# Kernel tuning notes

Hardware: AMD Instinct MI355X
Metric: run time of the kernel (lower is better)

Reference implementation:

```python
import jax, jax.numpy as jnp
import numpy as np

B, N, F, D, H, T = 32, 1024, 32, 64, 64, 4


def setup_inputs() -> dict:
    key = jax.random.key(0)
    ks = jax.random.split(key, 12)
    def w(k, shape):
        return 0.01 * jax.random.normal(k, shape, dtype=jnp.float32)
    z = lambda *s: jnp.zeros(s, jnp.float32)
    return {
        "xv": jax.random.normal(ks[0], (B, N, F), dtype=jnp.float32),
        "option": jax.random.uniform(ks[1], (B, 1), dtype=jnp.float32),
        "adj": jax.random.normal(ks[2], (N, N), dtype=jnp.float32),
        "mu1": w(ks[3], (F, D)),
        "W2": w(ks[4], (D, D)), "b2": z(D),
        "W3": w(ks[5], (D, D)), "b3": z(D),
        "W4": w(ks[6], (D, 1)), "b4": z(D),
        "Wq1": w(ks[7], (D, D)), "bq1": z(D),
        "Wq2": w(ks[8], (D, 1)), "bq2": z(D),
        "Wreg": w(ks[9], (H, 2 * D)), "breg": z(H),
        "Wq": w(ks[10], (1, H)), "bq": z(1),
    }


def reference(xv, option, adj, mu1, W2, b2, W3, b3, W4, b4,
              Wq1, bq1, Wq2, bq2, Wreg, breg, Wq, bq):
    # binary adjacency for message passing, raw weights for the mu_4 branch
    A = (adj > 0).astype(xv.dtype)                       # [N,N]
    mu_1 = jnp.maximum(xv @ mu1, 0.0)                    # [B,N,D]
    # mu_4: Linear(1,D) over every edge weight, clamp, sum over neighbors
    # (identical value every round t>=1, so computed once)
    mu4 = jnp.maximum(adj[..., None] * W4[:, 0] + b4, 0.0).sum(axis=1)[None]  # [1,N,D]
    mu3 = mu4 @ W3.T + b3                                # [1,N,D]
    mu = mu_1                                            # t = 0
    for _ in range(1, T):                                # t = 1..T-1
        mu_pool = jnp.einsum('nm,bmd->bnd', A, mu)       # neighbor aggregation
        mu2 = mu_pool @ W2.T + b2
        mu = jnp.maximum(mu_1 + mu2 + mu3, 0.0)
    mu_mean = jnp.maximum(mu.mean(axis=1, keepdims=True) @ Wq1.T + bq1, 0.0)  # [B,1,D]
    mu_aug = jnp.concatenate([mu, mu_mean], axis=1)      # [B,N+1,D]
    q2 = option.reshape(B, 1, 1) @ Wq2.T + bq2           # [B,1,D]
    q2 = jnp.broadcast_to(q2, (B, N + 1, D))
    q_ = jnp.concatenate([mu_aug, q2], axis=-1)          # [B,N+1,2D]
    qreg = jnp.maximum(q_ @ Wreg.T + breg, 0.0)          # [B,N+1,H]
    return qreg @ Wq.T + bq                              # [B,N+1,1]
```

## Files before the change

### kernel.cpp

```cpp
#include <hip/hip_runtime.h>
#include <hip/hip_bf16.h>

#define Bc 32
#define Nc 1024
#define Fc 32
#define Dc 64
#define Hc 64

typedef __bf16 bf16;
typedef __bf16 bf16x4 __attribute__((ext_vector_type(4)));
typedef __bf16 bf16x8 __attribute__((ext_vector_type(8)));
typedef float  f32x4  __attribute__((ext_vector_type(4)));

#define AS_STRIDE 136
#define MS_STRIDE 72

#define LDS_RND_NONF 26112
#define LDS_RND_FIN  27904

__global__ void k_pc(const float* __restrict__ adj, const float* __restrict__ W4,
                     const float* __restrict__ b4, const float* __restrict__ W3,
                     const float* __restrict__ b3, const float* __restrict__ b2,
                     const float* __restrict__ W2, const float* __restrict__ option,
                     const float* __restrict__ Wq2, const float* __restrict__ bq2,
                     const float* __restrict__ Wreg, const float* __restrict__ breg,
                     bf16* __restrict__ Abf, float* __restrict__ C3,
                     bf16* __restrict__ W2bf, float* __restrict__ c2base,
                     float* __restrict__ musum) {
    const int t = threadIdx.x;
    if (blockIdx.x < 1024) {
        const int n = blockIdx.x;
        const float* arow = adj + (size_t)n * Nc;
        {
            const float4 a = *(const float4*)&arow[t * 4];
            bf16x4 o;
            o[0] = (bf16)((a.x > 0.f) ? 1.f : 0.f);
            o[1] = (bf16)((a.y > 0.f) ? 1.f : 0.f);
            o[2] = (bf16)((a.z > 0.f) ? 1.f : 0.f);
            o[3] = (bf16)((a.w > 0.f) ? 1.f : 0.f);
            *(bf16x4*)&Abf[(size_t)n * Nc + t * 4] = o;
        }
        const int e = t & 63, g = t >> 6;
        __shared__ float red[256];
        __shared__ float mu4_s[64];
        const float w4e = W4[e], b4e = b4[e];
        float acc = 0.f;
        const float4* arow4 = (const float4*)(arow + g * 256);
#pragma unroll 8
        for (int j = 0; j < 64; ++j) {
            const float4 av = arow4[j];
            acc += fmaxf(fmaf(av.x, w4e, b4e), 0.f);
            acc += fmaxf(fmaf(av.y, w4e, b4e), 0.f);
            acc += fmaxf(fmaf(av.z, w4e, b4e), 0.f);
            acc += fmaxf(fmaf(av.w, w4e, b4e), 0.f);
        }
        red[t] = acc;
        __syncthreads();
        if (g == 0) mu4_s[e] = red[e] + red[64 + e] + red[128 + e] + red[192 + e];
        __syncthreads();
        if (t < 64) {
            const int d = t;
            float a = b3[d] + b2[d];
#pragma unroll
            for (int ee = 0; ee < 64; ++ee) a = fmaf(mu4_s[ee], W3[d * 64 + ee], a);
            C3[n * 64 + d] = a;
        }
    } else {
        for (int j = t * 16; j < t * 16 + 16; ++j) W2bf[j] = (bf16)W2[j];
        for (int i = t; i < 2048; i += 256) musum[i] = 0.f;
        for (int i = t; i < 2048; i += 256) {
            const int b = i >> 6, h = i & 63;
            const float opt = option[b];
            float a = breg[h];
#pragma unroll
            for (int j = 0; j < 64; ++j)
                a = fmaf(fmaf(opt, Wq2[j], bq2[j]), Wreg[h * 128 + 64 + j], a);
            c2base[i] = a;
        }
    }
}

__global__ void k_mu1(const float* __restrict__ xv, const float* __restrict__ w,
                      const bf16* __restrict__ W2bf,
                      float* __restrict__ mu_1, bf16* __restrict__ Xt) {
    const int nb = blockIdx.x, b = blockIdx.y, t = threadIdx.x;
    const int n0 = nb * 64;
    const int l = t & 63, wv = t >> 6, lm = l & 15, q = l >> 4;
    __shared__ bf16 xhi[64 * 40], xlo[64 * 40];
    __shared__ bf16 whi[64 * 40], wlo[64 * 40];
    __shared__ bf16 muS[64 * MS_STRIDE];
    __shared__ bf16 W2s[64 * MS_STRIDE];

    {
        const int row = t >> 2, f0 = (t & 3) * 8;
        const float* src = &xv[((size_t)b * Nc + n0 + row) * Fc + f0];
        const float4 v0 = *(const float4*)src;
        const float4 v1 = *(const float4*)(src + 4);
        bf16x8 hi, lo;
        float vv[8] = {v0.x, v0.y, v0.z, v0.w, v1.x, v1.y, v1.z, v1.w};
#pragma unroll
        for (int j = 0; j < 8; ++j) { hi[j] = (bf16)vv[j]; lo[j] = (bf16)(vv[j] - (float)hi[j]); }
        *(bf16x8*)&xhi[row * 40 + f0] = hi;
        *(bf16x8*)&xlo[row * 40 + f0] = lo;
    }
    {
        const int d = t >> 2, f0 = (t & 3) * 8;
#pragma unroll
        for (int j = 0; j < 8; ++j) {
            const float v = w[(f0 + j) * Dc + d];
            const bf16 hi = (bf16)v;
            whi[d * 40 + f0 + j] = hi;
            wlo[d * 40 + f0 + j] = (bf16)(v - (float)hi);
        }
    }
#pragma unroll
    for (int i = 0; i < 2; ++i) {
        int g = i * 256 + t, row = g >> 3, c = g & 7;
        *(bf16x8*)&W2s[row * MS_STRIDE + c * 8] = *(const bf16x8*)&W2bf[row * 64 + c * 8];
    }
    __syncthreads();

    f32x4 acc[4];
#pragma unroll
    for (int ct = 0; ct < 4; ++ct)
#pragma unroll
        for (int r = 0; r < 4; ++r) acc[ct][r] = 0.f;
    {
        const bf16x8 aHi = *(const bf16x8*)&xhi[(wv * 16 + lm) * 40 + q * 8];
        const bf16x8 aLo = *(const bf16x8*)&xlo[(wv * 16 + lm) * 40 + q * 8];
#pragma unroll
        for (int ct = 0; ct < 4; ++ct) {
            const bf16x8 bHi = *(const bf16x8*)&whi[(ct * 16 + lm) * 40 + q * 8];
            const bf16x8 bLo = *(const bf16x8*)&wlo[(ct * 16 + lm) * 40 + q * 8];
            acc[ct] = __builtin_amdgcn_mfma_f32_16x16x32_bf16(aHi, bHi, acc[ct], 0, 0, 0);
            acc[ct] = __builtin_amdgcn_mfma_f32_16x16x32_bf16(aLo, bHi, acc[ct], 0, 0, 0);
            acc[ct] = __builtin_amdgcn_mfma_f32_16x16x32_bf16(aHi, bLo, acc[ct], 0, 0, 0);
        }
    }
#pragma unroll
    for (int ct = 0; ct < 4; ++ct) {
        const int col = ct * 16 + lm;
#pragma unroll
        for (int r = 0; r < 4; ++r) {
            const int row = wv * 16 + q * 4 + r;
            const float v = fmaxf(acc[ct][r], 0.f);
            mu_1[((size_t)b * Nc + n0 + row) * Dc + col] = v;
            muS[row * MS_STRIDE + col] = (bf16)v;
        }
    }
    __syncthreads();
    f32x4 xacc[4];
#pragma unroll
    for (int ct = 0; ct < 4; ++ct)
#pragma unroll
        for (int r = 0; r < 4; ++r) xacc[ct][r] = 0.f;
#pragma unroll
    for (int s = 0; s < 2; ++s) {
        bf16x8 a = *(const bf16x8*)&muS[(wv * 16 + lm) * MS_STRIDE + s * 32 + q * 8];
#pragma unroll
        for (int ct = 0; ct < 4; ++ct) {
            bf16x8 bv = *(const bf16x8*)&W2s[(ct * 16 + lm) * MS_STRIDE + s * 32 + q * 8];
            xacc[ct] = __builtin_amdgcn_mfma_f32_16x16x32_bf16(a, bv, xacc[ct], 0, 0, 0);
        }
    }
#pragma unroll
    for (int ct = 0; ct < 4; ++ct) {
        const int dd = ct * 16 + lm;
        bf16x4 p;
#pragma unroll
        for (int r = 0; r < 4; ++r) p[r] = (bf16)xacc[ct][r];
        *(bf16x4*)&Xt[(size_t)b * 65536 + (size_t)dd * 1024 + n0 + wv * 16 + q * 4] = p;
    }
}

template <bool FINAL>
__global__ __launch_bounds__(256, 4)
void k_round(const bf16* __restrict__ Abf, const bf16* __restrict__ Xt_in,
             const float* __restrict__ mu_1, const float* __restrict__ C3,
             const bf16* __restrict__ W2bf, bf16* __restrict__ Xt_out,
             const float* __restrict__ Wreg, const float* __restrict__ c2base,
             const float* __restrict__ Wq, const float* __restrict__ bq,
             float* __restrict__ musum, float* __restrict__ out) {
    const int b = blockIdx.x, nb = blockIdx.y, t = threadIdx.x;
    const int n0 = nb * 32;
    const int l = t & 63, wv = t >> 6, lm = l & 15, q = l >> 4;
    const int rw = wv & 1, cth = wv >> 1;
    extern __shared__ char smem[];
    bf16* As   = (bf16*)smem;
    bf16* Xs   = (bf16*)(smem + 8704);
    bf16* muHi = (bf16*)smem;
    bf16* WHi  = (bf16*)(smem + 4608);
    bf16* muLo = (bf16*)(smem + 13824);
    bf16* WLo  = (bf16*)(smem + 18432);
    float* rpart = (float*)(smem + 27648);

    bf16x8 pw[2];
    bf16x4 wrhi[4], wrlo[4];
    if (!FINAL) {
#pragma unroll
        for (int i = 0; i < 2; ++i) {
            int g = i * 256 + t, row = g >> 3, c = g & 7;
            pw[i] = *(const bf16x8*)&W2bf[row * 64 + c * 8];
        }
    } else {
#pragma unroll
        for (int i = 0; i < 4; ++i) {
            int g = i * 1024 + t * 4;
            int h = g >> 6, d = g & 63;
            const float4 w4 = *(const float4*)&Wreg[h * 128 + d];
            wrhi[i][0] = (bf16)w4.x; wrlo[i][0] = (bf16)(w4.x - (float)wrhi[i][0]);
            wrhi[i][1] = (bf16)w4.y; wrlo[i][1] = (bf16)(w4.y - (float)wrhi[i][1]);
            wrhi[i][2] = (bf16)w4.z; wrlo[i][2] = (bf16)(w4.z - (float)wrhi[i][2]);
            wrhi[i][3] = (bf16)w4.w; wrlo[i][3] = (bf16)(w4.w - (float)wrhi[i][3]);
        }
    }

    f32x4 acc[2];
#pragma unroll
    for (int ct = 0; ct < 2; ++ct)
#pragma unroll
        for (int r = 0; r < 4; ++r) acc[ct][r] = 0.f;

    const bf16* Arow = Abf + (size_t)n0 * 1024;
    const bf16* Xrow = Xt_in + (size_t)b * 65536;

    bf16x8 pa[2], px[4];
#pragma unroll
    for (int i = 0; i < 2; ++i) {
        int g = i * 256 + t, row = g >> 4, c = g & 15;
        pa[i] = *(const bf16x8*)&Arow[(size_t)row * 1024 + c * 8];
    }
#pragma unroll
    for (int i = 0; i < 4; ++i) {
        int g = i * 256 + t, row = g >> 4, c = g & 15;
        px[i] = *(const bf16x8*)&Xrow[(size_t)row * 1024 + c * 8];
    }

    for (int kc = 0; kc < 1024; kc += 128) {
        __syncthreads();
#pragma unroll
        for (int i = 0; i < 2; ++i) {
            int g = i * 256 + t, row = g >> 4, c = g & 15;
            *(bf16x8*)&As[row * AS_STRIDE + c * 8] = pa[i];
        }
#pragma unroll
        for (int i = 0; i < 4; ++i) {
            int g = i * 256 + t, row = g >> 4, c = g & 15;
            *(bf16x8*)&Xs[row * AS_STRIDE + c * 8] = px[i];
        }
        __syncthreads();
        if (kc + 128 < 1024) {
#pragma unroll
            for (int i = 0; i < 2; ++i) {
                int g = i * 256 + t, row = g >> 4, c = g & 15;
                pa[i] = *(const bf16x8*)&Arow[(size_t)row * 1024 + kc + 128 + c * 8];
            }
#pragma unroll
            for (int i = 0; i < 4; ++i) {
                int g = i * 256 + t, row = g >> 4, c = g & 15;
                px[i] = *(const bf16x8*)&Xrow[(size_t)row * 1024 + kc + 128 + c * 8];
            }
        }
#pragma unroll
        for (int s = 0; s < 4; ++s) {
            bf16x8 a = *(const bf16x8*)&As[(rw * 16 + lm) * AS_STRIDE + s * 32 + q * 8];
#pragma unroll
            for (int ct = 0; ct < 2; ++ct) {
                bf16x8 bv = *(const bf16x8*)&Xs[(cth * 32 + ct * 16 + lm) * AS_STRIDE + s * 32 + q * 8];
                acc[ct] = __builtin_amdgcn_mfma_f32_16x16x32_bf16(a, bv, acc[ct], 0, 0, 0);
            }
        }
    }

    float vals[2][4];
#pragma unroll
    for (int ct = 0; ct < 2; ++ct) {
        const int col = cth * 32 + ct * 16 + lm;
#pragma unroll
        for (int r = 0; r < 4; ++r) {
            const int n = n0 + rw * 16 + q * 4 + r;
            float v = mu_1[((size_t)b * Nc + n) * Dc + col] + acc[ct][r] + C3[n * 64 + col];
            vals[ct][r] = fmaxf(v, 0.f);
        }
    }

    __syncthreads();
    if (!FINAL) {
#pragma unroll
        for (int i = 0; i < 2; ++i) {
            int g = i * 256 + t, row = g >> 3, c = g & 7;
            *(bf16x8*)&WHi[row * MS_STRIDE + c * 8] = pw[i];
        }
    } else {
#pragma unroll
        for (int i = 0; i < 4; ++i) {
            int g = i * 1024 + t * 4;
            int h = g >> 6, d = g & 63;
            *(bf16x4*)&WHi[h * MS_STRIDE + d] = wrhi[i];
            *(bf16x4*)&WLo[h * MS_STRIDE + d] = wrlo[i];
        }
    }
#pragma unroll
    for (int ct = 0; ct < 2; ++ct) {
        const int col = cth * 32 + ct * 16 + lm;
#pragma unroll
        for (int r = 0; r < 4; ++r) {
            const int row = rw * 16 + q * 4 + r;
            const float v = vals[ct][r];
            const bf16 hi = (bf16)v;
            muHi[row * MS_STRIDE + col] = hi;
            if (FINAL) muLo[row * MS_STRIDE + col] = (bf16)(v - (float)hi);
        }
    }
    if (FINAL) {
#pragma unroll
        for (int ct = 0; ct < 2; ++ct) {
            float s = vals[ct][0] + vals[ct][1] + vals[ct][2] + vals[ct][3];
            s += __shfl_xor(s, 16);
            s += __shfl_xor(s, 32);
            if (q == 0) atomicAdd(&musum[b * 64 + cth * 32 + ct * 16 + lm], s);
        }
    }
    __syncthreads();

    f32x4 xacc[2];
#pragma unroll
    for (int ct = 0; ct < 2; ++ct)
#pragma unroll
        for (int r = 0; r < 4; ++r) xacc[ct][r] = 0.f;

    if (!FINAL) {
#pragma unroll
        for (int s = 0; s < 2; ++s) {
            bf16x8 a = *(const bf16x8*)&muHi[(rw * 16 + lm) * MS_STRIDE + s * 32 + q * 8];
#pragma unroll
            for (int ct = 0; ct < 2; ++ct) {
                bf16x8 bv = *(const bf16x8*)&WHi[(cth * 32 + ct * 16 + lm) * MS_STRIDE + s * 32 + q * 8];
                xacc[ct] = __builtin_amdgcn_mfma_f32_16x16x32_bf16(a, bv, xacc[ct], 0, 0, 0);
            }
        }
#pragma unroll
        for (int ct = 0; ct < 2; ++ct) {
            const int dd = cth * 32 + ct * 16 + lm;
            bf16x4 p;
#pragma unroll
            for (int r = 0; r < 4; ++r) p[r] = (bf16)xacc[ct][r];
            *(bf16x4*)&Xt_out[(size_t)b * 65536 + (size_t)dd * 1024 + n0 + rw * 16 + q * 4] = p;
        }
    } else {
#pragma unroll
        for (int s = 0; s < 2; ++s) {
            const int aoff = (rw * 16 + lm) * MS_STRIDE + s * 32 + q * 8;
            bf16x8 aHi = *(const bf16x8*)&muHi[aoff];
            bf16x8 aLo = *(const bf16x8*)&muLo[aoff];
#pragma unroll
            for (int ct = 0; ct < 2; ++ct) {
                const int boff = (cth * 32 + ct * 16 + lm) * MS_STRIDE + s * 32 + q * 8;
                bf16x8 bHi = *(const bf16x8*)&WHi[boff];
                bf16x8 bLo = *(const bf16x8*)&WLo[boff];
                xacc[ct] = __builtin_amdgcn_mfma_f32_16x16x32_bf16(aHi, bHi, xacc[ct], 0, 0, 0);
                xacc[ct] = __builtin_amdgcn_mfma_f32_16x16x32_bf16(aLo, bHi, xacc[ct], 0, 0, 0);
                xacc[ct] = __builtin_amdgcn_mfma_f32_16x16x32_bf16(aHi, bLo, xacc[ct], 0, 0, 0);
            }
        }
        float rowsum[4] = {0.f, 0.f, 0.f, 0.f};
#pragma unroll
        for (int ct = 0; ct < 2; ++ct) {
            const int h = cth * 32 + ct * 16 + lm;
            const float c2 = c2base[b * 64 + h];
            const float wqh = Wq[h];
#pragma unroll
            for (int r = 0; r < 4; ++r)
                rowsum[r] += fmaxf(xacc[ct][r] + c2, 0.f) * wqh;
        }
#pragma unroll
        for (int r = 0; r < 4; ++r) {
            float v = rowsum[r];
            v += __shfl_xor(v, 1);
            v += __shfl_xor(v, 2);
            v += __shfl_xor(v, 4);
            v += __shfl_xor(v, 8);
            if (lm == 0) rpart[cth * 32 + rw * 16 + q * 4 + r] = v;
        }
        __syncthreads();
        if (t < 32)
            out[(size_t)b * (Nc + 1) + n0 + t] = rpart[t] + rpart[32 + t] + bq[0];
    }
}

__global__ void k_tail(const float* __restrict__ musum, const float* __restrict__ Wq1,
                       const float* __restrict__ bq1, const float* __restrict__ Wreg,
                       const float* __restrict__ c2base, const float* __restrict__ Wq,
                       const float* __restrict__ bq, float* __restrict__ out) {
    const int b = blockIdx.x, l = threadIdx.x;
    __shared__ float mean_s[64];
    __shared__ float mp[64];
    mean_s[l] = musum[b * 64 + l] * (1.f / Nc);
    __syncthreads();
    float a = bq1[l];
#pragma unroll
    for (int e = 0; e < 64; ++e) a = fmaf(mean_s[e], Wq1[l * 64 + e], a);
    mp[l] = fmaxf(a, 0.f);
    __syncthreads();
    float h = c2base[b * 64 + l];
#pragma unroll
    for (int d = 0; d < 64; ++d) h = fmaf(mp[d], Wreg[l * 128 + d], h);
    float v = fmaxf(h, 0.f) * Wq[l];
#pragma unroll
    for (int off = 32; off; off >>= 1) v += __shfl_down(v, off);
    if (l == 0) out[(size_t)b * (Nc + 1) + Nc] = v + bq[0];
}

extern "C" void kernel_launch(void* const* d_in, const int* in_sizes, int n_in,
                              void* d_out, int out_size, void* d_ws, size_t ws_size,
                              hipStream_t stream) {
    const float* xv     = (const float*)d_in[0];
    const float* option = (const float*)d_in[1];
    const float* adj    = (const float*)d_in[2];
    const float* mu1w   = (const float*)d_in[3];
    const float* W2     = (const float*)d_in[4];
    const float* b2     = (const float*)d_in[5];
    const float* W3     = (const float*)d_in[6];
    const float* b3     = (const float*)d_in[7];
    const float* W4     = (const float*)d_in[8];
    const float* b4     = (const float*)d_in[9];
    const float* Wq1    = (const float*)d_in[10];
    const float* bq1    = (const float*)d_in[11];
    const float* Wq2    = (const float*)d_in[12];
    const float* bq2    = (const float*)d_in[13];
    const float* Wreg   = (const float*)d_in[14];
    const float* breg   = (const float*)d_in[15];
    const float* Wq     = (const float*)d_in[16];
    const float* bq     = (const float*)d_in[17];
    float* out = (float*)d_out;

    float* ws = (float*)d_ws;
    const size_t MU = (size_t)Bc * Nc * Dc;
    float* mu_1     = ws;
    float* C3       = ws + MU;
    float* c2base   = C3 + 65536;
    float* musum    = c2base + 2048;
    bf16*  Abf      = (bf16*)(musum + 2048);
    bf16*  W2bf     = Abf + (size_t)Nc * Nc;
    bf16*  Xt0      = W2bf + 4096;
    bf16*  Xt1      = Xt0 + MU;

    k_pc<<<1025, 256, 0, stream>>>(adj, W4, b4, W3, b3, b2, W2, option, Wq2, bq2,
                                   Wreg, breg, Abf, C3, W2bf, c2base, musum);
    k_mu1<<<dim3(Nc / 64, Bc), 256, 0, stream>>>(xv, mu1w, W2bf, mu_1, Xt0);
    k_round<false><<<dim3(Bc, Nc / 32), 256, LDS_RND_NONF, stream>>>(
        Abf, Xt0, mu_1, C3, W2bf, Xt1,
        nullptr, nullptr, nullptr, nullptr, nullptr, nullptr);
    k_round<false><<<dim3(Bc, Nc / 32), 256, LDS_RND_NONF, stream>>>(
        Abf, Xt1, mu_1, C3, W2bf, Xt0,
        nullptr, nullptr, nullptr, nullptr, nullptr, nullptr);
    k_round<true><<<dim3(Bc, Nc / 32), 256, LDS_RND_FIN, stream>>>(
        Abf, Xt0, mu_1, C3, nullptr, nullptr,
        Wreg, c2base, Wq, bq, musum, out);
    k_tail<<<Bc, 64, 0, stream>>>(musum, Wq1, bq1, Wreg, c2base, Wq, bq, out);
}
```

Measured before the change: 159.3 us.

## Drop LDS staging in aggregation GEMM; load MFMA fragments directly with 64-row tiles

The round kernel no longer stages A and X tiles through shared memory with double-buffered register prefetch. Each wave now reads its MFMA fragments straight from global memory and computes a 2x2 block of 16x16 tiles. Block tile height doubles from 32 to 64 rows, which halves the grid and lowers the launch-bounds occupancy hint. The aim is to remove LDS round trips and barriers in the main loop, at the risk of uncoalesced global loads and lower occupancy.

```diff
diff --git a/kernel.cpp b/kernel.cpp
--- a/kernel.cpp
+++ b/kernel.cpp
@@ -12,11 +12,9 @@
 typedef __bf16 bf16x8 __attribute__((ext_vector_type(8)));
 typedef float  f32x4  __attribute__((ext_vector_type(4)));
 
-#define AS_STRIDE 136
-#define MS_STRIDE 72
-
-#define LDS_RND_NONF 26112
-#define LDS_RND_FIN  27904
+#define MS 72
+#define LDS_RND_NONF 18432
+#define LDS_RND_FIN  37376
 
 __global__ void k_pc(const float* __restrict__ adj, const float* __restrict__ W4,
                      const float* __restrict__ b4, const float* __restrict__ W3,
@@ -88,9 +86,8 @@
     const int l = t & 63, wv = t >> 6, lm = l & 15, q = l >> 4;
     __shared__ bf16 xhi[64 * 40], xlo[64 * 40];
     __shared__ bf16 whi[64 * 40], wlo[64 * 40];
-    __shared__ bf16 muS[64 * MS_STRIDE];
-    __shared__ bf16 W2s[64 * MS_STRIDE];
-
+    __shared__ bf16 muS[64 * MS];
+    __shared__ bf16 W2s[64 * MS];
     {
         const int row = t >> 2, f0 = (t & 3) * 8;
         const float* src = &xv[((size_t)b * Nc + n0 + row) * Fc + f0];
@@ -116,10 +113,9 @@
 #pragma unroll
     for (int i = 0; i < 2; ++i) {
         int g = i * 256 + t, row = g >> 3, c = g & 7;
-        *(bf16x8*)&W2s[row * MS_STRIDE + c * 8] = *(const bf16x8*)&W2bf[row * 64 + c * 8];
+        *(bf16x8*)&W2s[row * MS + c * 8] = *(const bf16x8*)&W2bf[row * 64 + c * 8];
     }
     __syncthreads();
-
     f32x4 acc[4];
 #pragma unroll
     for (int ct = 0; ct < 4; ++ct)
@@ -145,7 +141,7 @@
             const int row = wv * 16 + q * 4 + r;
             const float v = fmaxf(acc[ct][r], 0.f);
             mu_1[((size_t)b * Nc + n0 + row) * Dc + col] = v;
-            muS[row * MS_STRIDE + col] = (bf16)v;
+            muS[row * MS + col] = (bf16)v;
         }
     }
     __syncthreads();
@@ -156,10 +152,10 @@
         for (int r = 0; r < 4; ++r) xacc[ct][r] = 0.f;
 #pragma unroll
     for (int s = 0; s < 2; ++s) {
-        bf16x8 a = *(const bf16x8*)&muS[(wv * 16 + lm) * MS_STRIDE + s * 32 + q * 8];
+        bf16x8 a = *(const bf16x8*)&muS[(wv * 16 + lm) * MS + s * 32 + q * 8];
 #pragma unroll
         for (int ct = 0; ct < 4; ++ct) {
-            bf16x8 bv = *(const bf16x8*)&W2s[(ct * 16 + lm) * MS_STRIDE + s * 32 + q * 8];
+            bf16x8 bv = *(const bf16x8*)&W2s[(ct * 16 + lm) * MS + s * 32 + q * 8];
             xacc[ct] = __builtin_amdgcn_mfma_f32_16x16x32_bf16(a, bv, xacc[ct], 0, 0, 0);
         }
     }
@@ -174,7 +170,7 @@
 }
 
 template <bool FINAL>
-__global__ __launch_bounds__(256, 4)
+__global__ __launch_bounds__(256, 2)
 void k_round(const bf16* __restrict__ Abf, const bf16* __restrict__ Xt_in,
              const float* __restrict__ mu_1, const float* __restrict__ C3,
              const bf16* __restrict__ W2bf, bf16* __restrict__ Xt_out,
@@ -182,209 +178,197 @@
              const float* __restrict__ Wq, const float* __restrict__ bq,
              float* __restrict__ musum, float* __restrict__ out) {
     const int b = blockIdx.x, nb = blockIdx.y, t = threadIdx.x;
-    const int n0 = nb * 32;
+    const int n0 = nb * 64;
     const int l = t & 63, wv = t >> 6, lm = l & 15, q = l >> 4;
-    const int rw = wv & 1, cth = wv >> 1;
+    const int rh = wv & 1, ch = wv >> 1;
     extern __shared__ char smem[];
-    bf16* As   = (bf16*)smem;
-    bf16* Xs   = (bf16*)(smem + 8704);
     bf16* muHi = (bf16*)smem;
-    bf16* WHi  = (bf16*)(smem + 4608);
-    bf16* muLo = (bf16*)(smem + 13824);
-    bf16* WLo  = (bf16*)(smem + 18432);
-    float* rpart = (float*)(smem + 27648);
-
-    bf16x8 pw[2];
-    bf16x4 wrhi[4], wrlo[4];
+    bf16* muLo = (bf16*)(smem + 9216);
+    bf16* WHi  = (bf16*)(smem + (FINAL ? 18432 : 9216));
+    bf16* WLo  = (bf16*)(smem + 27648);
+    float* rpart = (float*)(smem + 36864);
+
     if (!FINAL) {
 #pragma unroll
         for (int i = 0; i < 2; ++i) {
             int g = i * 256 + t, row = g >> 3, c = g & 7;
-            pw[i] = *(const bf16x8*)&W2bf[row * 64 + c * 8];
+            *(bf16x8*)&WHi[row * MS + c * 8] = *(const bf16x8*)&W2bf[row * 64 + c * 8];
         }
     } else {
 #pragma unroll
         for (int i = 0; i < 4; ++i) {
-            int g = i * 1024 + t * 4;
-            int h = g >> 6, d = g & 63;
+            int g = i * 1024 + t * 4, h = g >> 6, d = g & 63;
             const float4 w4 = *(const float4*)&Wreg[h * 128 + d];
-            wrhi[i][0] = (bf16)w4.x; wrlo[i][0] = (bf16)(w4.x - (float)wrhi[i][0]);
-            wrhi[i][1] = (bf16)w4.y; wrlo[i][1] = (bf16)(w4.y - (float)wrhi[i][1]);
-            wrhi[i][2] = (bf16)w4.z; wrlo[i][2] = (bf16)(w4.z - (float)wrhi[i][2]);
-            wrhi[i][3] = (bf16)w4.w; wrlo[i][3] = (bf16)(w4.w - (float)wrhi[i][3]);
-        }
-    }
-
-    f32x4 acc[2];
-#pragma unroll
-    for (int ct = 0; ct < 2; ++ct)
-#pragma unroll
-        for (int r = 0; r < 4; ++r) acc[ct][r] = 0.f;
-
-    const bf16* Arow = Abf + (size_t)n0 * 1024;
-    const bf16* Xrow = Xt_in + (size_t)b * 65536;
-
-    bf16x8 pa[2], px[4];
-#pragma unroll
-    for (int i = 0; i < 2; ++i) {
-        int g = i * 256 + t, row = g >> 4, c = g & 15;
-        pa[i] = *(const bf16x8*)&Arow[(size_t)row * 1024 + c * 8];
-    }
-#pragma unroll
-    for (int i = 0; i < 4; ++i) {
-        int g = i * 256 + t, row = g >> 4, c = g & 15;
-        px[i] = *(const bf16x8*)&Xrow[(size_t)row * 1024 + c * 8];
-    }
-
-    for (int kc = 0; kc < 1024; kc += 128) {
-        __syncthreads();
-#pragma unroll
-        for (int i = 0; i < 2; ++i) {
-            int g = i * 256 + t, row = g >> 4, c = g & 15;
-            *(bf16x8*)&As[row * AS_STRIDE + c * 8] = pa[i];
-        }
-#pragma unroll
-        for (int i = 0; i < 4; ++i) {
-            int g = i * 256 + t, row = g >> 4, c = g & 15;
-            *(bf16x8*)&Xs[row * AS_STRIDE + c * 8] = px[i];
-        }
-        __syncthreads();
-        if (kc + 128 < 1024) {
-#pragma unroll
-            for (int i = 0; i < 2; ++i) {
-                int g = i * 256 + t, row = g >> 4, c = g & 15;
-                pa[i] = *(const bf16x8*)&Arow[(size_t)row * 1024 + kc + 128 + c * 8];
-            }
-#pragma unroll
-            for (int i = 0; i < 4; ++i) {
-                int g = i * 256 + t, row = g >> 4, c = g & 15;
-                px[i] = *(const bf16x8*)&Xrow[(size_t)row * 1024 + kc + 128 + c * 8];
-            }
-        }
-#pragma unroll
-        for (int s = 0; s < 4; ++s) {
-            bf16x8 a = *(const bf16x8*)&As[(rw * 16 + lm) * AS_STRIDE + s * 32 + q * 8];
-#pragma unroll
-            for (int ct = 0; ct < 2; ++ct) {
-                bf16x8 bv = *(const bf16x8*)&Xs[(cth * 32 + ct * 16 + lm) * AS_STRIDE + s * 32 + q * 8];
-                acc[ct] = __builtin_amdgcn_mfma_f32_16x16x32_bf16(a, bv, acc[ct], 0, 0, 0);
-            }
-        }
-    }
-
-    float vals[2][4];
-#pragma unroll
-    for (int ct = 0; ct < 2; ++ct) {
-        const int col = cth * 32 + ct * 16 + lm;
-#pragma unroll
-        for (int r = 0; r < 4; ++r) {
-            const int n = n0 + rw * 16 + q * 4 + r;
-            float v = mu_1[((size_t)b * Nc + n) * Dc + col] + acc[ct][r] + C3[n * 64 + col];
-            vals[ct][r] = fmaxf(v, 0.f);
-        }
-    }
-
-    __syncthreads();
-    if (!FINAL) {
-#pragma unroll
-        for (int i = 0; i < 2; ++i) {
-            int g = i * 256 + t, row = g >> 3, c = g & 7;
-            *(bf16x8*)&WHi[row * MS_STRIDE + c * 8] = pw[i];
-        }
-    } else {
-#pragma unroll
-        for (int i = 0; i < 4; ++i) {
-            int g = i * 1024 + t * 4;
-            int h = g >> 6, d = g & 63;
-            *(bf16x4*)&WHi[h * MS_STRIDE + d] = wrhi[i];
-            *(bf16x4*)&WLo[h * MS_STRIDE + d] = wrlo[i];
-        }
-    }
-#pragma unroll
-    for (int ct = 0; ct < 2; ++ct) {
-        const int col = cth * 32 + ct * 16 + lm;
-#pragma unroll
-        for (int r = 0; r < 4; ++r) {
-            const int row = rw * 16 + q * 4 + r;
-            const float v = vals[ct][r];
-            const bf16 hi = (bf16)v;
-            muHi[row * MS_STRIDE + col] = hi;
-            if (FINAL) muLo[row * MS_STRIDE + col] = (bf16)(v - (float)hi);
-        }
-    }
+            bf16x4 ohi, olo;
+            ohi[0] = (bf16)w4.x; olo[0] = (bf16)(w4.x - (float)ohi[0]);
+            ohi[1] = (bf16)w4.y; olo[1] = (bf16)(w4.y - (float)ohi[1]);
+            ohi[2] = (bf16)w4.z; olo[2] = (bf16)(w4.z - (float)ohi[2]);
+            ohi[3] = (bf16)w4.w; olo[3] = (bf16)(w4.w - (float)ohi[3]);
+            *(bf16x4*)&WHi[h * MS + d] = ohi;
+            *(bf16x4*)&WLo[h * MS + d] = olo;
+        }
+    }
+
+    f32x4 acc[2][2];
+#pragma unroll
+    for (int rt = 0; rt < 2; ++rt)
+#pragma unroll
+        for (int ct = 0; ct < 2; ++ct)
+#pragma unroll
+            for (int r = 0; r < 4; ++r) acc[rt][ct][r] = 0.f;
+
+    const bf16* Ab0 = Abf + (size_t)(n0 + rh * 32 + lm) * 1024 + q * 8;
+    const bf16* Ab1 = Ab0 + 16 * 1024;
+    const bf16* Xb0 = Xt_in + (size_t)b * 65536 + (size_t)(ch * 32 + lm) * 1024 + q * 8;
+    const bf16* Xb1 = Xb0 + 16 * 1024;
+#pragma unroll 4
+    for (int s = 0; s < 32; ++s) {
+        const int o = s * 32;
+        bf16x8 a0 = *(const bf16x8*)&Ab0[o];
+        bf16x8 a1 = *(const bf16x8*)&Ab1[o];
+        bf16x8 x0 = *(const bf16x8*)&Xb0[o];
+        bf16x8 x1 = *(const bf16x8*)&Xb1[o];
+        acc[0][0] = __builtin_amdgcn_mfma_f32_16x16x32_bf16(a0, x0, acc[0][0], 0, 0, 0);
+        acc[0][1] = __builtin_amdgcn_mfma_f32_16x16x32_bf16(a0, x1, acc[0][1], 0, 0, 0);
+        acc[1][0] = __builtin_amdgcn_mfma_f32_16x16x32_bf16(a1, x0, acc[1][0], 0, 0, 0);
+        acc[1][1] = __builtin_amdgcn_mfma_f32_16x16x32_bf16(a1, x1, acc[1][1], 0, 0, 0);
+    }
+
+    float vals[2][2][4];
+#pragma unroll
+    for (int rt = 0; rt < 2; ++rt)
+#pragma unroll
+        for (int ct = 0; ct < 2; ++ct) {
+            const int col = ch * 32 + ct * 16 + lm;
+#pragma unroll
+            for (int r = 0; r < 4; ++r) {
+                const int n = n0 + rh * 32 + rt * 16 + q * 4 + r;
+                float v = mu_1[((size_t)b * Nc + n) * Dc + col] + acc[rt][ct][r]
+                        + C3[n * 64 + col];
+                vals[rt][ct][r] = fmaxf(v, 0.f);
+            }
+        }
+
+#pragma unroll
+    for (int rt = 0; rt < 2; ++rt)
+#pragma unroll
+        for (int ct = 0; ct < 2; ++ct) {
+            const int col = ch * 32 + ct * 16 + lm;
+#pragma unroll
+            for (int r = 0; r < 4; ++r) {
+                const int row = rh * 32 + rt * 16 + q * 4 + r;
+                const float v = vals[rt][ct][r];
+                const bf16 hi = (bf16)v;
+                muHi[row * MS + col] = hi;
+                if (FINAL) muLo[row * MS + col] = (bf16)(v - (float)hi);
+            }
+        }
     if (FINAL) {
 #pragma unroll
         for (int ct = 0; ct < 2; ++ct) {
-            float s = vals[ct][0] + vals[ct][1] + vals[ct][2] + vals[ct][3];
+            float s = 0.f;
+#pragma unroll
+            for (int rt = 0; rt < 2; ++rt)
+#pragma unroll
+                for (int r = 0; r < 4; ++r) s += vals[rt][ct][r];
             s += __shfl_xor(s, 16);
             s += __shfl_xor(s, 32);
-            if (q == 0) atomicAdd(&musum[b * 64 + cth * 32 + ct * 16 + lm], s);
+            if (q == 0) atomicAdd(&musum[b * 64 + ch * 32 + ct * 16 + lm], s);
         }
     }
     __syncthreads();
 
-    f32x4 xacc[2];
-#pragma unroll
-    for (int ct = 0; ct < 2; ++ct)
-#pragma unroll
-        for (int r = 0; r < 4; ++r) xacc[ct][r] = 0.f;
+    f32x4 xacc[2][2];
+#pragma unroll
+    for (int rt = 0; rt < 2; ++rt)
+#pragma unroll
+        for (int ct = 0; ct < 2; ++ct)
+#pragma unroll
+            for (int r = 0; r < 4; ++r) xacc[rt][ct][r] = 0.f;
 
     if (!FINAL) {
 #pragma unroll
         for (int s = 0; s < 2; ++s) {
-            bf16x8 a = *(const bf16x8*)&muHi[(rw * 16 + lm) * MS_STRIDE + s * 32 + q * 8];
+            bf16x8 aM[2], bW[2];
+#pragma unroll
+            for (int rt = 0; rt < 2; ++rt)
+                aM[rt] = *(const bf16x8*)&muHi[(rh * 32 + rt * 16 + lm) * MS + s * 32 + q * 8];
+#pragma unroll
+            for (int ct = 0; ct < 2; ++ct)
+                bW[ct] = *(const bf16x8*)&WHi[(ch * 32 + ct * 16 + lm) * MS + s * 32 + q * 8];
+#pragma unroll
+            for (int rt = 0; rt < 2; ++rt)
+#pragma unroll
+                for (int ct = 0; ct < 2; ++ct)
+                    xacc[rt][ct] = __builtin_amdgcn_mfma_f32_16x16x32_bf16(aM[rt], bW[ct],
+                                                                           xacc[rt][ct], 0, 0, 0);
+        }
+#pragma unroll
+        for (int rt = 0; rt < 2; ++rt)
 #pragma unroll
             for (int ct = 0; ct < 2; ++ct) {
-                bf16x8 bv = *(const bf16x8*)&WHi[(cth * 32 + ct * 16 + lm) * MS_STRIDE + s * 32 + q * 8];
-                xacc[ct] = __builtin_amdgcn_mfma_f32_16x16x32_bf16(a, bv, xacc[ct], 0, 0, 0);
-            }
-        }
+                const int dd = ch * 32 + ct * 16 + lm;
+                bf16x4 p;
+#pragma unroll
+                for (int r = 0; r < 4; ++r) p[r] = (bf16)xacc[rt][ct][r];
+                *(bf16x4*)&Xt_out[(size_t)b * 65536 + (size_t)dd * 1024
+                                  + n0 + rh * 32 + rt * 16 + q * 4] = p;
+            }
+    } else {
+#pragma unroll
+        for (int s = 0; s < 2; ++s) {
+            bf16x8 aH[2], aL[2], bH[2], bL[2];
+#pragma unroll
+            for (int rt = 0; rt < 2; ++rt) {
+                const int ao = (rh * 32 + rt * 16 + lm) * MS + s * 32 + q * 8;
+                aH[rt] = *(const bf16x8*)&muHi[ao];
+                aL[rt] = *(const bf16x8*)&muLo[ao];
+            }
+#pragma unroll
+            for (int ct = 0; ct < 2; ++ct) {
+                const int bo = (ch * 32 + ct * 16 + lm) * MS + s * 32 + q * 8;
+                bH[ct] = *(const bf16x8*)&WHi[bo];
+                bL[ct] = *(const bf16x8*)&WLo[bo];
+            }
+#pragma unroll
+            for (int rt = 0; rt < 2; ++rt)
+#pragma unroll
+                for (int ct = 0; ct < 2; ++ct) {
+                    xacc[rt][ct] = __builtin_amdgcn_mfma_f32_16x16x32_bf16(aH[rt], bH[ct],
+                                                                           xacc[rt][ct], 0, 0, 0);
+                    xacc[rt][ct] = __builtin_amdgcn_mfma_f32_16x16x32_bf16(aL[rt], bH[ct],
+                                                                           xacc[rt][ct], 0, 0, 0);
+                    xacc[rt][ct] = __builtin_amdgcn_mfma_f32_16x16x32_bf16(aH[rt], bL[ct],
+                                                                           xacc[rt][ct], 0, 0, 0);
+                }
+        }
+        const float bq0 = bq[0];
+        float rowsum[2][4] = {{0.f, 0.f, 0.f, 0.f}, {0.f, 0.f, 0.f, 0.f}};
 #pragma unroll
         for (int ct = 0; ct < 2; ++ct) {
-            const int dd = cth * 32 + ct * 16 + lm;
-            bf16x4 p;
-#pragma unroll
-            for (int r = 0; r < 4; ++r) p[r] = (bf16)xacc[ct][r];
-            *(bf16x4*)&Xt_out[(size_t)b * 65536 + (size_t)dd * 1024 + n0 + rw * 16 + q * 4] = p;
-        }
-    } else {
-#pragma unroll
-        for (int s = 0; s < 2; ++s) {
-            const int aoff = (rw * 16 + lm) * MS_STRIDE + s * 32 + q * 8;
-            bf16x8 aHi = *(const bf16x8*)&muHi[aoff];
-            bf16x8 aLo = *(const bf16x8*)&muLo[aoff];
-#pragma unroll
-            for (int ct = 0; ct < 2; ++ct) {
-                const int boff = (cth * 32 + ct * 16 + lm) * MS_STRIDE + s * 32 + q * 8;
-                bf16x8 bHi = *(const bf16x8*)&WHi[boff];
-                bf16x8 bLo = *(const bf16x8*)&WLo[boff];
-                xacc[ct] = __builtin_amdgcn_mfma_f32_16x16x32_bf16(aHi, bHi, xacc[ct], 0, 0, 0);
-                xacc[ct] = __builtin_amdgcn_mfma_f32_16x16x32_bf16(aLo, bHi, xacc[ct], 0, 0, 0);
-                xacc[ct] = __builtin_amdgcn_mfma_f32_16x16x32_bf16(aHi, bLo, xacc[ct], 0, 0, 0);
-            }
-        }
-        float rowsum[4] = {0.f, 0.f, 0.f, 0.f};
-#pragma unroll
-        for (int ct = 0; ct < 2; ++ct) {
-            const int h = cth * 32 + ct * 16 + lm;
+            const int h = ch * 32 + ct * 16 + lm;
             const float c2 = c2base[b * 64 + h];
             const float wqh = Wq[h];
 #pragma unroll
-            for (int r = 0; r < 4; ++r)
-                rowsum[r] += fmaxf(xacc[ct][r] + c2, 0.f) * wqh;
-        }
-#pragma unroll
-        for (int r = 0; r < 4; ++r) {
-            float v = rowsum[r];
-            v += __shfl_xor(v, 1);
-            v += __shfl_xor(v, 2);
-            v += __shfl_xor(v, 4);
-            v += __shfl_xor(v, 8);
-            if (lm == 0) rpart[cth * 32 + rw * 16 + q * 4 + r] = v;
-        }
+            for (int rt = 0; rt < 2; ++rt)
+#pragma unroll
+                for (int r = 0; r < 4; ++r)
+                    rowsum[rt][r] += fmaxf(xacc[rt][ct][r] + c2, 0.f) * wqh;
+        }
+#pragma unroll
+        for (int rt = 0; rt < 2; ++rt)
+#pragma unroll
+            for (int r = 0; r < 4; ++r) {
+                float v = rowsum[rt][r];
+                v += __shfl_xor(v, 1);
+                v += __shfl_xor(v, 2);
+                v += __shfl_xor(v, 4);
+                v += __shfl_xor(v, 8);
+                if (lm == 0) rpart[ch * 64 + rh * 32 + rt * 16 + q * 4 + r] = v;
+            }
         __syncthreads();
-        if (t < 32)
-            out[(size_t)b * (Nc + 1) + n0 + t] = rpart[t] + rpart[32 + t] + bq[0];
+        if (t < 64)
+            out[(size_t)b * (Nc + 1) + n0 + t] = rpart[t] + rpart[64 + t] + bq0;
     }
 }
 
@@ -448,13 +432,13 @@
     k_pc<<<1025, 256, 0, stream>>>(adj, W4, b4, W3, b3, b2, W2, option, Wq2, bq2,
                                    Wreg, breg, Abf, C3, W2bf, c2base, musum);
     k_mu1<<<dim3(Nc / 64, Bc), 256, 0, stream>>>(xv, mu1w, W2bf, mu_1, Xt0);
-    k_round<false><<<dim3(Bc, Nc / 32), 256, LDS_RND_NONF, stream>>>(
+    k_round<false><<<dim3(Bc, 16), 256, LDS_RND_NONF, stream>>>(
         Abf, Xt0, mu_1, C3, W2bf, Xt1,
         nullptr, nullptr, nullptr, nullptr, nullptr, nullptr);
-    k_round<false><<<dim3(Bc, Nc / 32), 256, LDS_RND_NONF, stream>>>(
+    k_round<false><<<dim3(Bc, 16), 256, LDS_RND_NONF, stream>>>(
         Abf, Xt1, mu_1, C3, W2bf, Xt0,
         nullptr, nullptr, nullptr, nullptr, nullptr, nullptr);
-    k_round<true><<<dim3(Bc, Nc / 32), 256, LDS_RND_FIN, stream>>>(
+    k_round<true><<<dim3(Bc, 16), 256, LDS_RND_FIN, stream>>>(
         Abf, Xt0, mu_1, C3, nullptr, nullptr,
         Wreg, c2base, Wq, bq, musum, out);
     k_tail<<<Bc, 64, 0, stream>>>(musum, Wq1, bq1, Wreg, c2base, Wq, bq, out);
```

After: 215.1 us. 35.0% more time.
